# Performance work log

Hardware: AMD Instinct MI355X
Metric: run time of the kernel (lower is better)

## Reference

```python
import jax, jax.numpy as jnp
import numpy as np

B, S, D, HD, P = 4, 8192, 1024, 128, 32
EPS_LN = 1e-5

def setup_inputs() -> dict:
    key = jax.random.key(0)
    ks = jax.random.split(key, 12)
    x      = jax.random.normal(ks[0], (B, S, D), dtype=jnp.float32)
    W_proj = jax.random.normal(ks[1], (8, D, HD), dtype=jnp.float32) * 0.02
    freqs  = jax.random.normal(ks[2], (8, HD), dtype=jnp.float32) * 0.01
    W_pol  = jax.random.normal(ks[3], (8, HD, P), dtype=jnp.float32) * 0.05
    b_pol  = jnp.zeros((8, P), jnp.float32)
    W_imp1 = jax.random.normal(ks[4], (1, 16), dtype=jnp.float32) * 0.5
    b_imp1 = jnp.zeros((16,), jnp.float32)
    W_imp2 = jax.random.normal(ks[5], (16, 1), dtype=jnp.float32) * 0.5
    b_imp2 = jnp.zeros((1,), jnp.float32)
    W_out  = jax.random.normal(ks[6], (D, D), dtype=jnp.float32) * 0.02
    b_out  = jnp.zeros((D,), jnp.float32)
    gamma  = jnp.ones((D,), jnp.float32)
    beta   = jnp.zeros((D,), jnp.float32)
    return dict(x=x, W_proj=W_proj, freqs=freqs, W_pol=W_pol, b_pol=b_pol,
                W_imp1=W_imp1, b_imp1=b_imp1, W_imp2=W_imp2, b_imp2=b_imp2,
                W_out=W_out, b_out=b_out, gamma=gamma, beta=beta)

def reference(x, W_proj, freqs, W_pol, b_pol, W_imp1, b_imp1, W_imp2, b_imp2,
              W_out, b_out, gamma, beta):
    # heads[i] = (x @ W_proj[i]) * cos(pi * freqs[i])   -> (8, B, S, HD)
    heads = jnp.einsum('bsd,hde->hbse', x, W_proj) * jnp.cos(freqs * jnp.pi)[:, None, None, :]

    # --- GuaXiangDuiChong: impedance matrix (B, 8, 8) ---
    hm = heads.mean(axis=2)                                   # (8, B, HD)
    pv = jnp.tanh(jnp.einsum('hbd,hdp->bhp', hm, W_pol) + b_pol[None])  # (B, 8, P)
    pm = pv / jnp.maximum(jnp.linalg.norm(pv, axis=-1, keepdims=True), 1e-12)
    dp = jnp.einsum('bhp,bgp->bhg', pm, pm)                   # (B, 8, 8)
    z = jax.nn.gelu(dp[..., None] * W_imp1[0] + b_imp1, approximate=False)  # (B,8,8,16)
    imp = jax.nn.softplus(jnp.einsum('bhgk,ko->bhgo', z, W_imp2)[..., 0] + b_imp2[0])
    imp = imp * (1.0 - jnp.eye(8, dtype=imp.dtype))           # zero diagonal

    # --- head mixing. Causal masked-mean collapses to row scale (s+1)/S ---
    coeff = (0.1 / (1.0 + imp)) * (1.0 - jnp.eye(8, dtype=imp.dtype))  # (B,8,8), j!=i
    mix = jnp.einsum('big,gbsd->ibsd', coeff, heads)          # (8, B, S, HD)
    causal_scale = (jnp.arange(S, dtype=x.dtype) + 1.0) / S   # (S,)
    out_heads = heads + causal_scale[None, None, :, None] * mix

    merged = out_heads.transpose(1, 2, 0, 3).reshape(B, S, D)
    proj = jnp.einsum('bsd,de->bse', merged, W_out) + b_out   # dropout = identity (eval)
    y = proj + x
    mu = y.mean(axis=-1, keepdims=True)
    var = y.var(axis=-1, keepdims=True)
    y = (y - mu) * jax.lax.rsqrt(var + EPS_LN) * gamma + beta
    return y, imp
```

## Files before the change

### kernel.cpp

```cpp
#include <hip/hip_runtime.h>
#include <hip/hip_bf16.h>
#include <math.h>

typedef __bf16 bf16;
typedef __bf16 bf16x2 __attribute__((ext_vector_type(2)));
typedef __bf16 bf16x4 __attribute__((ext_vector_type(4)));
typedef __bf16 bf16x8 __attribute__((ext_vector_type(8)));
typedef float  f32x4  __attribute__((ext_vector_type(4)));

#define NB 4
#define SS 8192
#define DD 1024
#define MM 32768
#define KK 1024
#define NN 1024
#define PI_F 3.14159265358979323846f

__device__ __forceinline__ void gl2lds16(const bf16* g, bf16* l) {
    __builtin_amdgcn_global_load_lds(
        (const __attribute__((address_space(1))) void*)g,
        (__attribute__((address_space(3))) void*)l, 16, 0, 0);
}

__global__ __launch_bounds__(256) void prep_all(const float* __restrict__ x,
                                                bf16* __restrict__ xb,
                                                const float* __restrict__ W_proj,
                                                const float* __restrict__ freqs,
                                                const float* __restrict__ W_out,
                                                bf16* __restrict__ WbT1,
                                                bf16* __restrict__ WoT,
                                                float* __restrict__ hm) {
    int blk = blockIdx.x;
    if (blk < MM) {
        size_t i = (size_t)blk * 1024 + threadIdx.x * 4;
        float4 v = *(const float4*)&x[i];
        bf16x4 o;
        o[0] = (bf16)v.x; o[1] = (bf16)v.y; o[2] = (bf16)v.z; o[3] = (bf16)v.w;
        *(bf16x4*)&xb[i] = o;
    } else {
        int idx = (blk - MM) * 256 + threadIdx.x;
        int n = idx >> 10, k = idx & 1023;
        int h = n >> 7, d = n & 127;
        float c = cosf(PI_F * freqs[n]);
        WbT1[idx] = (bf16)(W_proj[(size_t)h * (DD * 128) + (size_t)k * 128 + d] * c);
        WoT[idx]  = (bf16)(W_out[(size_t)k * DD + n]);
        if (idx < NB * DD) hm[idx] = 0.0f;
    }
}


#define FENCE  asm volatile("" ::: "memory")
#define BARRIER do { FENCE; __builtin_amdgcn_s_barrier(); FENCE; } while (0)
#define PRIO1  __builtin_amdgcn_s_setprio(1)
#define PRIO0  __builtin_amdgcn_s_setprio(0)
#define VMC(N) asm volatile("s_waitcnt vmcnt(" #N ")" ::: "memory")
#define NOPS   ((void)0)

#define STG(g0, g1, uk, ldsBase)                                  \
    gl2lds16((g0) + (uk), &sm[(ldsBase) + w * 512]);              \
    gl2lds16((g1) + (uk), &sm[(ldsBase) + 4096 + w * 512]);

#define READ_A2(MQ, ab)                                                          \
    _Pragma("unroll") for (int m_ = 0; m_ < 4; ++m_) {                           \
        a[m_ * 2 + 0] = *(const bf16x8*)&sm[(ab) + aoff0 + ((MQ)*64 + m_*16)*64];\
        a[m_ * 2 + 1] = *(const bf16x8*)&sm[(ab) + aoff1 + ((MQ)*64 + m_*16)*64];\
    }
#define READ_B2(NQ, bfr, bb)                                                     \
    _Pragma("unroll") for (int n_ = 0; n_ < 2; ++n_) {                           \
        bfr[n_ * 2 + 0] = *(const bf16x8*)&sm[(bb) + boff0 + ((NQ)*32 + n_*16)*64];\
        bfr[n_ * 2 + 1] = *(const bf16x8*)&sm[(bb) + boff1 + ((NQ)*32 + n_*16)*64];\
    }

#define MFMA_Q(MQ, NQ, bfr)                                                    \
    _Pragma("unroll") for (int m_ = 0; m_ < 4; ++m_)                           \
    _Pragma("unroll") for (int n_ = 0; n_ < 2; ++n_)                           \
    _Pragma("unroll") for (int ks_ = 0; ks_ < 2; ++ks_)                        \
        acc[(MQ) * 4 + m_][(NQ) * 2 + n_] =                                    \
            __builtin_amdgcn_mfma_f32_16x16x32_bf16(                           \
                a[m_ * 2 + ks_], bfr[n_ * 2 + ks_],                            \
                acc[(MQ) * 4 + m_][(NQ) * 2 + n_], 0, 0, 0);

#define ITER(uk1, STG3, STG4, STG5, STG6, STG7, STG8, VM4, VM8)                \
  {                                                                    \
    BARRIER; STG(gA00, gA01, (uk1), 16384);                                    \
    PRIO1; READ_A2(0, 0); READ_B2(0, blo, 32768);                              \
    MFMA_Q(0, 0, blo); PRIO0;                                                  \
                                                                       \
    BARRIER; STG(gA10, gA11, (uk1), 24576);                                    \
    PRIO1; READ_B2(1, bhi, 32768); MFMA_Q(0, 1, bhi); PRIO0;                   \
                                                                       \
    BARRIER; STG3;                                                             \
    PRIO1; READ_A2(1, 0); MFMA_Q(1, 1, bhi); PRIO0;                            \
                                                     \
    BARRIER; STG4; VM4;                                                        \
    PRIO1; MFMA_Q(1, 0, blo); PRIO0;                                           \
                                                                       \
    BARRIER; STG5;                                                             \
    PRIO1; READ_A2(0, 16384); READ_B2(0, blo, 49152);                          \
    MFMA_Q(0, 0, blo); PRIO0;                                                  \
                                                                       \
    BARRIER; STG6;                                                             \
    PRIO1; READ_B2(1, bhi, 49152); MFMA_Q(0, 1, bhi); PRIO0;                   \
                                                                       \
    BARRIER; STG7;                                                             \
    PRIO1; READ_A2(1, 16384); MFMA_Q(1, 1, bhi); PRIO0;                        \
                                                     \
    BARRIER; STG8; VM8;                                                        \
    PRIO1; MFMA_Q(1, 0, blo); PRIO0;                                           \
  }

template <int MODE>
__global__ __launch_bounds__(512, 2)
void gemm256(const bf16* __restrict__ A, int lda, const bf16* __restrict__ Bt,
             bf16* __restrict__ Cstr, const bf16* __restrict__ residb,
             const float* __restrict__ bias, float* __restrict__ hm) {
    __shared__ bf16 sm[65536];
    const int tid = threadIdx.x;
    const int lane = tid & 63, w = tid >> 6;
    const int wr = w >> 2, wc = w & 3;
    const int l15 = lane & 15, l4 = lane >> 4;

    int wg = blockIdx.x;
    int swz = (wg & 7) * 64 + (wg >> 3);
    const int mt = swz >> 2, ntile = swz & 3;
    const int row0 = mt * 256, col0 = ntile * 256;

    const int aoff0 = (wr * 128 + l15) * 64 + ((l4 ^ (l15 & 7)) << 3);
    const int aoff1 = aoff0 ^ 32;
    const int boff0 = (wc * 64 + l15) * 64 + ((l4 ^ (l15 & 7)) << 3);
    const int boff1 = boff0 ^ 32;

    const int srow = tid >> 3;
    const int scb  = (tid & 7) ^ (srow & 7);
    const bf16* gA00 = A + (size_t)(row0 + srow) * lda + scb * 8;
    const bf16* gA01 = gA00 + (size_t)64 * lda;
    const bf16* gA10 = gA00 + (size_t)128 * lda;
    const bf16* gA11 = gA00 + (size_t)192 * lda;
    const bf16* gB00 = Bt + (size_t)(col0 + srow) * 1024 + scb * 8;
    const bf16* gB01 = gB00 + 64 * 1024;
    const bf16* gB10 = gB00 + 128 * 1024;
    const bf16* gB11 = gB00 + 192 * 1024;

    f32x4 acc[8][4] = {};
    bf16x8 a[8], blo[4], bhi[4];

    STG(gA00, gA01, 0,  0);     STG(gA10, gA11, 0,  8192);
    STG(gB00, gB01, 0,  32768); STG(gB10, gB11, 0,  40960);
    STG(gA00, gA01, 64, 16384); STG(gA10, gA11, 64, 24576);
    STG(gB00, gB01, 64, 49152); STG(gB10, gB11, 64, 57344);
    VMC(0);

#pragma unroll 1
    for (int i = 0; i < 7; ++i) {
        const int uk1 = (2 * i + 1) * 64;
        const int uk2 = (2 * i + 2) * 64;
        const int uk3 = (2 * i + 3) * 64;
        ITER(uk1,
             STG(gB00, gB01, uk2, 32768), STG(gB10, gB11, uk2, 40960),
             STG(gA00, gA01, uk2, 0),     STG(gA10, gA11, uk2, 8192),
             STG(gB00, gB01, uk3, 49152), STG(gB10, gB11, uk3, 57344),
             VMC(4), VMC(4));
    }
    ITER(960, NOPS, NOPS, NOPS, NOPS, NOPS, NOPS, VMC(0), NOPS);

    if (MODE == 0) {
        const int batch = row0 >> 13;
#pragma unroll
        for (int mg = 0; mg < 8; ++mg) {
            int rbase = row0 + wr * 128 + (mg >> 2) * 64 + (mg & 3) * 16 + l4 * 4;
#pragma unroll
            for (int j = 0; j < 4; ++j) {
                size_t row = rbase + j;
#pragma unroll
                for (int ng = 0; ng < 4; ++ng) {
                    int col = col0 + wc * 64 + ng * 16 + l15;
                    Cstr[row * 2048 + col] = (bf16)acc[mg][ng][j];
                }
            }
        }
#pragma unroll
        for (int ng = 0; ng < 4; ++ng) {
            float s = 0;
#pragma unroll
            for (int mg = 0; mg < 8; ++mg)
#pragma unroll
                for (int j = 0; j < 4; ++j) s += acc[mg][ng][j];
            int col = col0 + wc * 64 + ng * 16 + l15;
            atomicAdd(&hm[batch * DD + col], s);
        }
    } else {
        float bi[4];
#pragma unroll
        for (int ng = 0; ng < 4; ++ng) bi[ng] = bias[col0 + wc * 64 + ng * 16 + l15];
#pragma unroll
        for (int mg = 0; mg < 8; ++mg) {
            int rbase = row0 + wr * 128 + (mg >> 2) * 64 + (mg & 3) * 16 + l4 * 4;
#pragma unroll
            for (int j = 0; j < 4; ++j) {
                size_t row = rbase + j;
#pragma unroll
                for (int ng = 0; ng < 4; ++ng) {
                    int col = col0 + wc * 64 + ng * 16 + l15;
                    Cstr[row * 2048 + col] =
                        (bf16)(acc[mg][ng][j] + bi[ng] + (float)residb[row * 1024 + col]);
                }
            }
        }
    }
}

__global__ __launch_bounds__(1024) void imp_k(const float* __restrict__ hm,
                                              const float* __restrict__ W_pol,
                                              const float* __restrict__ b_pol,
                                              const float* __restrict__ W_imp1,
                                              const float* __restrict__ b_imp1,
                                              const float* __restrict__ W_imp2,
                                              const float* __restrict__ b_imp2,
                                              float* __restrict__ imp_out,
                                              float* __restrict__ coeff) {
    __shared__ float pm_s[32][32];
    int tid = threadIdx.x;
    int bh = tid >> 5, p = tid & 31;
    int b = bh >> 3, h = bh & 7;
    float a = b_pol[h * 32 + p];
    for (int d = 0; d < 128; ++d)
        a += hm[b * DD + h * 128 + d] * (1.0f / SS) * W_pol[(h * 128 + d) * 32 + p];
    float pv = tanhf(a);
    pm_s[bh][p] = pv;
    __syncthreads();
    float ss = 0;
    for (int q = 0; q < 32; ++q) ss += pm_s[bh][q] * pm_s[bh][q];
    float pmv = pv / fmaxf(sqrtf(ss), 1e-12f);
    __syncthreads();
    pm_s[bh][p] = pmv;
    __syncthreads();
    if (tid < 256) {
        int b2 = tid >> 6, h2 = (tid >> 3) & 7, g = tid & 7;
        float dp = 0;
        for (int q = 0; q < 32; ++q) dp += pm_s[b2 * 8 + h2][q] * pm_s[b2 * 8 + g][q];
        float a2 = 0;
        for (int kk = 0; kk < 16; ++kk) {
            float zin = dp * W_imp1[kk] + b_imp1[kk];
            float zg = 0.5f * zin * (1.0f + erff(zin * 0.70710678118654752f));
            a2 += zg * W_imp2[kk];
        }
        float spin = a2 + b_imp2[0];
        float impv = (spin > 20.0f) ? spin : log1pf(expf(spin));
        if (h2 == g) impv = 0.0f;
        imp_out[tid] = impv;
        coeff[tid] = (h2 == g) ? 0.0f : 0.1f / (1.0f + impv);
    }
}

__global__ __launch_bounds__(256) void mix_k(const char* __restrict__ slots,
                                             const float* __restrict__ coeff,
                                             char* __restrict__ slots_w) {
    __shared__ float cf[64];
    int tid = threadIdx.x;
    size_t r0 = (size_t)blockIdx.x * 4;
    int b = (int)(r0 >> 13);
    if (tid < 64) cf[tid] = coeff[b * 64 + tid];
    __syncthreads();
    int lr = tid >> 6;
    int d2 = tid & 63;
    size_t r = r0 + lr;
    int s = (int)(r & (SS - 1));
    float cs = (float)(s + 1) * (1.0f / SS);
    const bf16* hrow = (const bf16*)(slots + r * 4096);
    bf16* mrow = (bf16*)(slots_w + r * 4096 + 2048);
    float v0[8], v1[8];
#pragma unroll
    for (int g = 0; g < 8; ++g) {
        bf16x2 v = *(const bf16x2*)&hrow[g * 128 + d2 * 2];
        v0[g] = (float)v[0]; v1[g] = (float)v[1];
    }
#pragma unroll
    for (int h = 0; h < 8; ++h) {
        float a0 = 0, a1 = 0;
#pragma unroll
        for (int g = 0; g < 8; ++g) {
            float c = cf[h * 8 + g];
            a0 += c * v0[g]; a1 += c * v1[g];
        }
        bf16x2 o;
        o[0] = (bf16)(v0[h] + cs * a0);
        o[1] = (bf16)(v1[h] + cs * a1);
        *(bf16x2*)&mrow[h * 128 + d2 * 2] = o;
    }
}

__global__ __launch_bounds__(256) void ln_k(char* __restrict__ slots,
                                            const float* __restrict__ gamma,
                                            const float* __restrict__ beta) {
    size_t r = blockIdx.x;
    int tid = threadIdx.x;
    const bf16* zrow = (const bf16*)(slots + r * 4096);
    float* yrow = (float*)(slots + r * 4096);
    int e0 = tid * 4;
    bf16x4 zv = *(const bf16x4*)&zrow[e0];
    float vx = (float)zv[0], vy = (float)zv[1], vz = (float)zv[2], vw = (float)zv[3];
    float sum = vx + vy + vz + vw;
    float sq  = vx * vx + vy * vy + vz * vz + vw * vw;
    for (int off = 32; off > 0; off >>= 1) {
        sum += __shfl_down(sum, off);
        sq  += __shfl_down(sq, off);
    }
    __shared__ float red[8];
    int lane = tid & 63, wv = tid >> 6;
    if (lane == 0) { red[wv] = sum; red[4 + wv] = sq; }
    __syncthreads();
    float tot = red[0] + red[1] + red[2] + red[3];
    float tsq = red[4] + red[5] + red[6] + red[7];
    float mu  = tot * (1.0f / DD);
    float var = tsq * (1.0f / DD) - mu * mu;
    float rs  = rsqrtf(var + 1e-5f);
    float4 g4 = *(const float4*)&gamma[e0];
    float4 b4 = *(const float4*)&beta[e0];
    float4 o;
    o.x = (vx - mu) * rs * g4.x + b4.x;
    o.y = (vy - mu) * rs * g4.y + b4.y;
    o.z = (vz - mu) * rs * g4.z + b4.z;
    o.w = (vw - mu) * rs * g4.w + b4.w;
    *(float4*)&yrow[e0] = o;
}

extern "C" void kernel_launch(void* const* d_in, const int* in_sizes, int n_in,
                              void* d_out, int out_size, void* d_ws, size_t ws_size,
                              hipStream_t stream) {
    const float* x      = (const float*)d_in[0];
    const float* W_proj = (const float*)d_in[1];
    const float* freqs  = (const float*)d_in[2];
    const float* W_pol  = (const float*)d_in[3];
    const float* b_pol  = (const float*)d_in[4];
    const float* W_imp1 = (const float*)d_in[5];
    const float* b_imp1 = (const float*)d_in[6];
    const float* W_imp2 = (const float*)d_in[7];
    const float* b_imp2 = (const float*)d_in[8];
    const float* W_out  = (const float*)d_in[9];
    const float* b_out  = (const float*)d_in[10];
    const float* gamma  = (const float*)d_in[11];
    const float* beta   = (const float*)d_in[12];

    char* ws = (char*)d_ws;
    bf16* xb     = (bf16*)ws;
    bf16* WbT1   = (bf16*)(ws + ((size_t)64 << 20));
    bf16* WoT    = (bf16*)(ws + ((size_t)66 << 20));
    float* hm    = (float*)(ws + ((size_t)68 << 20));
    float* coeff = (float*)(ws + ((size_t)68 << 20) + 16384);

    char* slots = (char*)d_out;
    float* imp_out = (float*)d_out + (size_t)MM * DD;

    prep_all<<<MM + 4096, 256, 0, stream>>>(x, xb, W_proj, freqs, W_out,
                                            WbT1, WoT, hm);

    gemm256<0><<<512, 512, 0, stream>>>(xb, 1024, WbT1, (bf16*)slots,
                                        nullptr, nullptr, hm);

    imp_k<<<1, 1024, 0, stream>>>(hm, W_pol, b_pol, W_imp1, b_imp1, W_imp2, b_imp2,
                                  imp_out, coeff);

    mix_k<<<MM / 4, 256, 0, stream>>>(slots, coeff, slots);

    gemm256<1><<<512, 512, 0, stream>>>((const bf16*)slots + 1024, 2048, WoT,
                                        (bf16*)slots, xb, b_out, nullptr);

    ln_k<<<MM, 256, 0, stream>>>(slots, gamma, beta);
}
```

Before: 266.1 us.

## Restructure GEMM pipeline into four phases and widen prep and mix vectorization

The GEMM main loop drops from eight barrier-separated phases to four. Each phase now issues two staging loads and reads both B halves at once. The prologue stops preloading the second A stage and waits with vmcnt(4) instead of draining all loads. Separately, prep_all converts 8 floats per thread instead of 4, and mix_k handles 16 rows per block with 16-byte bf16x8 loads and stores in place of bf16x2. These changes aim to cut barrier count and per-instruction memory overhead, at the risk of exposing load latency and raising register pressure in the GEMM and mix kernels.

```diff
diff --git a/kernel.cpp b/kernel.cpp
--- a/kernel.cpp
+++ b/kernel.cpp
@@ -31,14 +31,16 @@
                                                 bf16* __restrict__ WoT,
                                                 float* __restrict__ hm) {
     int blk = blockIdx.x;
-    if (blk < MM) {
-        size_t i = (size_t)blk * 1024 + threadIdx.x * 4;
-        float4 v = *(const float4*)&x[i];
-        bf16x4 o;
-        o[0] = (bf16)v.x; o[1] = (bf16)v.y; o[2] = (bf16)v.z; o[3] = (bf16)v.w;
-        *(bf16x4*)&xb[i] = o;
+    if (blk < MM / 2) {
+        size_t i = (size_t)blk * 2048 + threadIdx.x * 8;
+        float4 v0 = *(const float4*)&x[i];
+        float4 v1 = *(const float4*)&x[i + 4];
+        bf16x8 o;
+        o[0] = (bf16)v0.x; o[1] = (bf16)v0.y; o[2] = (bf16)v0.z; o[3] = (bf16)v0.w;
+        o[4] = (bf16)v1.x; o[5] = (bf16)v1.y; o[6] = (bf16)v1.z; o[7] = (bf16)v1.w;
+        *(bf16x8*)&xb[i] = o;
     } else {
-        int idx = (blk - MM) * 256 + threadIdx.x;
+        int idx = (blk - MM / 2) * 256 + threadIdx.x;
         int n = idx >> 10, k = idx & 1023;
         int h = n >> 7, d = n & 127;
         float c = cosf(PI_F * freqs[n]);
@@ -80,33 +82,25 @@
                 a[m_ * 2 + ks_], bfr[n_ * 2 + ks_],                            \
                 acc[(MQ) * 4 + m_][(NQ) * 2 + n_], 0, 0, 0);
 
-#define ITER(uk1, STG3, STG4, STG5, STG6, STG7, STG8, VM4, VM8)                \
-  {                                                                    \
-    BARRIER; STG(gA00, gA01, (uk1), 16384);                                    \
-    PRIO1; READ_A2(0, 0); READ_B2(0, blo, 32768);                              \
-    MFMA_Q(0, 0, blo); PRIO0;                                                  \
-                                                                       \
-    BARRIER; STG(gA10, gA11, (uk1), 24576);                                    \
-    PRIO1; READ_B2(1, bhi, 32768); MFMA_Q(0, 1, bhi); PRIO0;                   \
-                                                                       \
-    BARRIER; STG3;                                                             \
-    PRIO1; READ_A2(1, 0); MFMA_Q(1, 1, bhi); PRIO0;                            \
-                                                     \
-    BARRIER; STG4; VM4;                                                        \
-    PRIO1; MFMA_Q(1, 0, blo); PRIO0;                                           \
-                                                                       \
-    BARRIER; STG5;                                                             \
-    PRIO1; READ_A2(0, 16384); READ_B2(0, blo, 49152);                          \
-    MFMA_Q(0, 0, blo); PRIO0;                                                  \
-                                                                       \
-    BARRIER; STG6;                                                             \
-    PRIO1; READ_B2(1, bhi, 49152); MFMA_Q(0, 1, bhi); PRIO0;                   \
-                                                                       \
-    BARRIER; STG7;                                                             \
-    PRIO1; READ_A2(1, 16384); MFMA_Q(1, 1, bhi); PRIO0;                        \
-                                                     \
-    BARRIER; STG8; VM8;                                                        \
-    PRIO1; MFMA_Q(1, 0, blo); PRIO0;                                           \
+#define ITER(uk1, STGB2a, STGB2b, STGA2a, STGA2b, STGB3a, STGB3b, VM2, VM4)    \
+  {                        \
+    BARRIER;                                                                   \
+    STG(gA00, gA01, (uk1), 16384); STG(gA10, gA11, (uk1), 24576);              \
+    PRIO1; READ_A2(0, 0); READ_B2(0, blo, 32768); READ_B2(1, bhi, 32768);      \
+    MFMA_Q(0, 0, blo); MFMA_Q(0, 1, bhi); PRIO0;                               \
+                          \
+    BARRIER;                                                                   \
+    STGB2a; STGB2b; VM2;                                                       \
+    PRIO1; READ_A2(1, 0); MFMA_Q(1, 1, bhi); MFMA_Q(1, 0, blo); PRIO0;         \
+                         \
+    BARRIER;                                                                   \
+    STGA2a; STGA2b;                                                            \
+    PRIO1; READ_A2(0, 16384); READ_B2(0, blo, 49152); READ_B2(1, bhi, 49152);  \
+    MFMA_Q(0, 0, blo); MFMA_Q(0, 1, bhi); PRIO0;                               \
+                          \
+    BARRIER;                                                                   \
+    STGB3a; STGB3b; VM4;                                                       \
+    PRIO1; READ_A2(1, 16384); MFMA_Q(1, 1, bhi); MFMA_Q(1, 0, blo); PRIO0;     \
   }
 
 template <int MODE>
@@ -146,9 +140,8 @@
 
     STG(gA00, gA01, 0,  0);     STG(gA10, gA11, 0,  8192);
     STG(gB00, gB01, 0,  32768); STG(gB10, gB11, 0,  40960);
-    STG(gA00, gA01, 64, 16384); STG(gA10, gA11, 64, 24576);
     STG(gB00, gB01, 64, 49152); STG(gB10, gB11, 64, 57344);
-    VMC(0);
+    VMC(4);
 
 #pragma unroll 1
     for (int i = 0; i < 7; ++i) {
@@ -257,35 +250,34 @@
                                              char* __restrict__ slots_w) {
     __shared__ float cf[64];
     int tid = threadIdx.x;
-    size_t r0 = (size_t)blockIdx.x * 4;
+    size_t r0 = (size_t)blockIdx.x * 16;
     int b = (int)(r0 >> 13);
     if (tid < 64) cf[tid] = coeff[b * 64 + tid];
     __syncthreads();
-    int lr = tid >> 6;
-    int d2 = tid & 63;
-    size_t r = r0 + lr;
+    size_t r = r0 + (tid >> 4);
+    int dd = tid & 15;
     int s = (int)(r & (SS - 1));
     float cs = (float)(s + 1) * (1.0f / SS);
     const bf16* hrow = (const bf16*)(slots + r * 4096);
     bf16* mrow = (bf16*)(slots_w + r * 4096 + 2048);
-    float v0[8], v1[8];
+    float v[8][8];
 #pragma unroll
     for (int g = 0; g < 8; ++g) {
-        bf16x2 v = *(const bf16x2*)&hrow[g * 128 + d2 * 2];
-        v0[g] = (float)v[0]; v1[g] = (float)v[1];
+        bf16x8 t8 = *(const bf16x8*)&hrow[g * 128 + dd * 8];
+#pragma unroll
+        for (int e = 0; e < 8; ++e) v[g][e] = (float)t8[e];
     }
 #pragma unroll
     for (int h = 0; h < 8; ++h) {
-        float a0 = 0, a1 = 0;
-#pragma unroll
-        for (int g = 0; g < 8; ++g) {
-            float c = cf[h * 8 + g];
-            a0 += c * v0[g]; a1 += c * v1[g];
-        }
-        bf16x2 o;
-        o[0] = (bf16)(v0[h] + cs * a0);
-        o[1] = (bf16)(v1[h] + cs * a1);
-        *(bf16x2*)&mrow[h * 128 + d2 * 2] = o;
+        bf16x8 o;
+#pragma unroll
+        for (int e = 0; e < 8; ++e) {
+            float acc = 0;
+#pragma unroll
+            for (int g = 0; g < 8; ++g) acc += cf[h * 8 + g] * v[g][e];
+            o[e] = (bf16)(v[h][e] + cs * acc);
+        }
+        *(bf16x8*)&mrow[h * 128 + dd * 8] = o;
     }
 }
 
@@ -351,8 +343,8 @@
     char* slots = (char*)d_out;
     float* imp_out = (float*)d_out + (size_t)MM * DD;
 
-    prep_all<<<MM + 4096, 256, 0, stream>>>(x, xb, W_proj, freqs, W_out,
-                                            WbT1, WoT, hm);
+    prep_all<<<MM / 2 + 4096, 256, 0, stream>>>(x, xb, W_proj, freqs, W_out,
+                                                WbT1, WoT, hm);
 
     gemm256<0><<<512, 512, 0, stream>>>(xb, 1024, WbT1, (bf16*)slots,
                                         nullptr, nullptr, hm);
@@ -360,7 +352,7 @@
     imp_k<<<1, 1024, 0, stream>>>(hm, W_pol, b_pol, W_imp1, b_imp1, W_imp2, b_imp2,
                                   imp_out, coeff);
 
-    mix_k<<<MM / 4, 256, 0, stream>>>(slots, coeff, slots);
+    mix_k<<<MM / 16, 256, 0, stream>>>(slots, coeff, slots);
 
     gemm256<1><<<512, 512, 0, stream>>>((const bf16*)slots + 1024, 2048, WoT,
                                         (bf16*)slots, xb, b_out, nullptr);
```

Result: slower. 272.3 us (+2.3%).
